# Optimization experiments

Measured on AMD Instinct MI355X. Metric: run time of the kernel, lower is better.

## Reference

```python
import jax, jax.numpy as jnp
import numpy as np
from jax import lax

B = 16384
BN_EPS = 1e-5


def setup_inputs() -> dict:
    key = jax.random.key(0)
    ks = jax.random.split(key, 6)
    x = jax.random.normal(ks[0], (B, 1, 28, 28), jnp.float32)
    conv_w = jax.random.normal(ks[1], (4, 1, 3, 3), jnp.float32) * 0.2
    bn_gamma = jnp.ones((4,), jnp.float32)
    bn_beta = jnp.zeros((4,), jnp.float32)
    bn_mean = jnp.zeros((4,), jnp.float32)
    bn_var = jnp.ones((4,), jnp.float32)
    var_params = jax.random.normal(ks[2], (4,), jnp.float32)
    lin_w = jax.random.normal(ks[3], (10, 784), jnp.float32) * 0.03
    lin_b = jnp.zeros((10,), jnp.float32)
    return {"x": x, "conv_w": conv_w, "bn_gamma": bn_gamma, "bn_beta": bn_beta,
            "bn_mean": bn_mean, "bn_var": bn_var, "var_params": var_params,
            "lin_w": lin_w, "lin_b": lin_b}


def _ry_w0(s, theta):
    # apply RY(theta) to wire 0 (axis -2) of real state s[..., 2, 2]
    c, si = jnp.cos(theta * 0.5), jnp.sin(theta * 0.5)
    R = jnp.stack([jnp.stack([c, -si]), jnp.stack([si, c])])
    return jnp.einsum('ij,...jk->...ik', R, s)


def _ry_w1(s, theta):
    # apply RY(theta) to wire 1 (axis -1)
    c, si = jnp.cos(theta * 0.5), jnp.sin(theta * 0.5)
    R = jnp.stack([jnp.stack([c, -si]), jnp.stack([si, c])])
    return jnp.einsum('ij,...kj->...ki', R, s)


def _quantum_features(img, v):
    # img: [B, 28, 28] -> features [B, 196*4] (patch-major, 4 expvals each)
    b = img.shape[0]
    p = img.reshape(b, 14, 2, 14, 2).transpose(0, 1, 3, 2, 4)  # [B,14,14,2,2]
    # encoding RYs on same wire compose: angles a = p0+p2 (wire0), b = p1+p3 (wire1)
    ha = (p[..., 0, 0] + p[..., 1, 0]) * 0.5
    hb = (p[..., 0, 1] + p[..., 1, 1]) * 0.5
    w0 = jnp.stack([jnp.cos(ha), jnp.sin(ha)], axis=-1)
    w1 = jnp.stack([jnp.cos(hb), jnp.sin(hb)], axis=-1)
    s = w0[..., :, None] * w1[..., None, :]  # real statevector [B,14,14,2,2]
    # CNOT(control=0, target=1): flip wire1 where wire0 == 1
    s = jnp.stack([s[..., 0, :], s[..., 1, ::-1]], axis=-2)
    s = _ry_w0(s, v[0])
    s = _ry_w1(s, v[1])
    # CNOT(control=1, target=0): flip wire0 where wire1 == 1
    s = jnp.stack([s[..., :, 0], s[..., ::-1, 1]], axis=-1)
    s = _ry_w0(s, v[2])
    s = _ry_w1(s, v[3])
    z0 = jnp.sum(s[..., 0, :] ** 2 - s[..., 1, :] ** 2, axis=-1)
    z1 = jnp.sum(s[..., :, 0] ** 2 - s[..., :, 1] ** 2, axis=-1)
    x0 = 2.0 * jnp.sum(s[..., 0, :] * s[..., 1, :], axis=-1)
    x1 = 2.0 * jnp.sum(s[..., :, 0] * s[..., :, 1], axis=-1)
    return jnp.stack([z0, z1, x0, x1], axis=-1).reshape(b, -1)  # [B,784]


def reference(x, conv_w, bn_gamma, bn_beta, bn_mean, bn_var, var_params, lin_w, lin_b):
    b = x.shape[0]
    # classical branch: conv(s=2,p=1) -> BN (eval) -> ReLU -> flatten
    h = lax.conv_general_dilated(x, conv_w, window_strides=(2, 2),
                                 padding=((1, 1), (1, 1)))  # [B,4,14,14]
    inv = bn_gamma / jnp.sqrt(bn_var + BN_EPS)
    h = h * inv[None, :, None, None] + (bn_beta - bn_mean * inv)[None, :, None, None]
    h = jnp.maximum(h, 0.0)
    cls_out = h.reshape(b, -1)  # [B,784]
    # quantum branch over 2x2 patches
    q_out = _quantum_features(x[:, 0], var_params)  # [B,784]
    fused = cls_out + q_out
    logits = fused @ lin_w.T + lin_b
    return jax.nn.log_softmax(logits, axis=-1)
```

## Files before the change

kernel.cpp:

```cpp
#include <hip/hip_runtime.h>
#include <math.h>


#define NW 4
#define SCLS_STRIDE 794

typedef __fp16 h2 __attribute__((ext_vector_type(2)));
typedef __fp16 h4 __attribute__((ext_vector_type(4)));

#if __has_builtin(__builtin_amdgcn_fdot2)
#define FDOT2(a, b, c) __builtin_amdgcn_fdot2((a), (b), (c), false)
#else
__device__ __forceinline__ float FDOT2(h2 a, h2 b, float c) {
    return (float)a.x * (float)b.x + (float)a.y * (float)b.y + c;
}
#endif

__device__ __forceinline__ float2 red32x2(float x) {
    int v;
    v = __builtin_amdgcn_update_dpp(0, __float_as_int(x), 0x111, 0xf, 0xf, true); x += __int_as_float(v);
    v = __builtin_amdgcn_update_dpp(0, __float_as_int(x), 0x112, 0xf, 0xf, true); x += __int_as_float(v);
    v = __builtin_amdgcn_update_dpp(0, __float_as_int(x), 0x114, 0xf, 0xf, true); x += __int_as_float(v);
    v = __builtin_amdgcn_update_dpp(0, __float_as_int(x), 0x118, 0xf, 0xf, true); x += __int_as_float(v);
    v = __builtin_amdgcn_update_dpp(0, __float_as_int(x), 0x142, 0xa, 0xf, true); x += __int_as_float(v);
    float2 r;
    r.x = __int_as_float(__builtin_amdgcn_readlane(__float_as_int(x), 31));
    r.y = __int_as_float(__builtin_amdgcn_readlane(__float_as_int(x), 63));
    return r;
}

__global__ __launch_bounds__(256, 4)
void quanv_fused(const float* __restrict__ x,
                 const float* __restrict__ conv_w,
                 const float* __restrict__ bn_gamma,
                 const float* __restrict__ bn_beta,
                 const float* __restrict__ bn_mean,
                 const float* __restrict__ bn_var,
                 const float* __restrict__ var_params,
                 const float* __restrict__ lin_w,
                 const float* __restrict__ lin_b,
                 float* __restrict__ out, int B)
{
    __shared__ __align__(16) __fp16 lwh[7840];
    __shared__ __align__(16) __fp16 sclsAll[NW * 2 * SCLS_STRIDE];

    const int tid  = threadIdx.x;
    const int wave = tid >> 6;
    const int lane = tid & 63;
    const int half = lane >> 5;
    const int l32  = lane & 31;

    const int s  = blockIdx.x * (NW * 2) + wave * 2 + half;
    const int sc = (s < B) ? s : (B - 1);
    const float* xs = x + (size_t)sc * 784;
    __fp16* myscls = &sclsAll[(wave * 2 + half) * SCLS_STRIDE];

    {
        const float4* src = (const float4*)lin_w;
        #pragma unroll
        for (int t = 0; t < 8; ++t) {
            int i = tid + t * 256;
            if (i < 1960) {
                float4 v = src[i];
                h2 a = __builtin_amdgcn_cvt_pkrtz(v.x, v.y);
                h2 b = __builtin_amdgcn_cvt_pkrtz(v.z, v.w);
                h4 w4 = { a.x, a.y, b.x, b.y };
                *(h4*)&lwh[4 * i] = w4;
            }
        }
    }

    float w[36];
    #pragma unroll
    for (int k = 0; k < 36; ++k) w[k] = conv_w[k];
    float inv[4], addc[4];
    #pragma unroll
    for (int c = 0; c < 4; ++c) {
        float iv = bn_gamma[c] * rsqrtf(bn_var[c] + 1e-5f);
        inv[c]  = iv;
        addc[c] = bn_beta[c] - bn_mean[c] * iv;
    }
    float cv[4], sv[4];
    #pragma unroll
    for (int k = 0; k < 4; ++k) __sincosf(var_params[k] * 0.5f, &sv[k], &cv[k]);

    h2 qh[7][2];
    #pragma unroll
    for (int t = 0; t < 7; ++t) {
        int p = l32 + 32 * t;
        bool act = (p < 196);
        int pc = act ? p : 195;
        unsigned i = (unsigned)pc / 14u;
        int j = pc - (int)i * 14;
        int omid = (int)(2 * i) * 28 + 2 * j;

        float2 Rm = *(const float2*)(xs + omid);
        float2 Rb = *(const float2*)(xs + omid + 28);
        int ot = omid - 28; ot = (ot > 0) ? ot : 0;
        float2 Rt = *(const float2*)(xs + ot);
        int olt = omid - 30; olt = (olt > 0) ? olt : 0;
        float2 Lt = *(const float2*)(xs + olt);
        int olm = omid - 2; olm = (olm > 0) ? olm : 0;
        float2 Lm = *(const float2*)(xs + olm);
        float2 Lb = *(const float2*)(xs + olm + 28);

        float mt = (i > 0) ? 1.f : 0.f;
        float ml = (j > 0) ? 1.f : 0.f;
        float a00 = Lt.y * (mt * ml), a01 = Rt.x * mt, a02 = Rt.y * mt;
        float a10 = Lm.y * ml,        a11 = Rm.x,      a12 = Rm.y;
        float a20 = Lb.y * ml,        a21 = Rb.x,      a22 = Rb.y;

        if (act) {
            #pragma unroll
            for (int c = 0; c < 4; ++c) {
                float h = w[c*9+0]*a00 + w[c*9+1]*a01 + w[c*9+2]*a02
                        + w[c*9+3]*a10 + w[c*9+4]*a11 + w[c*9+5]*a12
                        + w[c*9+6]*a20 + w[c*9+7]*a21 + w[c*9+8]*a22;
                h = h * inv[c] + addc[c];
                myscls[c * 196 + pc] = (__fp16)fmaxf(h, 0.f);
            }
        }

        float ha = 0.5f * (a11 + a21);
        float hb = 0.5f * (a12 + a22);
        float c0, s0, c1, s1;
        __sincosf(ha, &s0, &c0);
        __sincosf(hb, &s1, &c1);
        float m00 = c0*c1, m01 = c0*s1;
        float m10 = s0*s1, m11 = s0*c1;
        float t00 = cv[0]*m00 - sv[0]*m10, t01 = cv[0]*m01 - sv[0]*m11;
        float t10 = sv[0]*m00 + cv[0]*m10, t11 = sv[0]*m01 + cv[0]*m11;
        float u00 = cv[1]*t00 - sv[1]*t01, u01 = sv[1]*t00 + cv[1]*t01;
        float u10 = cv[1]*t10 - sv[1]*t11, u11 = sv[1]*t10 + cv[1]*t11;
        float tmp = u01; u01 = u11; u11 = tmp;
        float p00 = cv[2]*u00 - sv[2]*u10, p01 = cv[2]*u01 - sv[2]*u11;
        float p10 = sv[2]*u00 + cv[2]*u10, p11 = sv[2]*u01 + cv[2]*u11;
        float q00 = cv[3]*p00 - sv[3]*p01, q01 = sv[3]*p00 + cv[3]*p01;
        float q10 = cv[3]*p10 - sv[3]*p11, q11 = sv[3]*p10 + cv[3]*p11;

        float z0 = q00*q00 + q01*q01 - q10*q10 - q11*q11;
        float z1 = q00*q00 + q10*q10 - q01*q01 - q11*q11;
        float x0 = 2.f * (q00*q10 + q01*q11);
        float x1 = 2.f * (q00*q01 + q10*q11);
        qh[t][0] = __builtin_amdgcn_cvt_pkrtz(z0, z1);
        qh[t][1] = __builtin_amdgcn_cvt_pkrtz(x0, x1);
    }

    __syncthreads();

    float ps[10];
    #pragma unroll
    for (int o = 0; o < 10; ++o) ps[o] = 0.f;

    const h2 hz = { (__fp16)0.f, (__fp16)0.f };
    #pragma unroll
    for (int t = 0; t < 7; ++t) {
        int p = l32 + 32 * t;
        bool act = (p < 196);
        int pc = act ? p : 195;
        h2 c0 = *(const h2*)&myscls[4 * pc];
        h2 c1 = *(const h2*)&myscls[4 * pc + 2];
        h2 f0 = c0 + qh[t][0];
        h2 f1 = c1 + qh[t][1];
        f0 = act ? f0 : hz;
        f1 = act ? f1 : hz;
        const __fp16* wbase = &lwh[4 * pc];
        #pragma unroll
        for (int o = 0; o < 10; ++o) {
            h4 wv = *(const h4*)&wbase[o * 784];
            h2 wlo = __builtin_shufflevector(wv, wv, 0, 1);
            h2 whi = __builtin_shufflevector(wv, wv, 2, 3);
            ps[o] = FDOT2(f0, wlo, ps[o]);
            ps[o] = FDOT2(f1, whi, ps[o]);
        }
    }

    float lg[10];
    #pragma unroll
    for (int o = 0; o < 10; ++o) {
        float2 r = red32x2(ps[o]);
        lg[o] = (half ? r.y : r.x) + lin_b[o];
    }

    float mx = lg[0];
    #pragma unroll
    for (int o = 1; o < 10; ++o) mx = fmaxf(mx, lg[o]);
    float se = 0.f;
    #pragma unroll
    for (int o = 0; o < 10; ++o) se += __expf(lg[o] - mx);
    float ls = __logf(se);

    int o32 = l32;
    if (o32 < 10 && s < B) {
        float v = lg[0];
        #pragma unroll
        for (int o = 1; o < 10; ++o) v = (o32 == o) ? lg[o] : v;
        out[(size_t)s * 10 + o32] = v - mx - ls;
    }
}

extern "C" void kernel_launch(void* const* d_in, const int* in_sizes, int n_in,
                              void* d_out, int out_size, void* d_ws, size_t ws_size,
                              hipStream_t stream) {
    const float* x          = (const float*)d_in[0];
    const float* conv_w     = (const float*)d_in[1];
    const float* bn_gamma   = (const float*)d_in[2];
    const float* bn_beta    = (const float*)d_in[3];
    const float* bn_mean    = (const float*)d_in[4];
    const float* bn_var     = (const float*)d_in[5];
    const float* var_params = (const float*)d_in[6];
    const float* lin_w      = (const float*)d_in[7];
    const float* lin_b      = (const float*)d_in[8];
    float* out = (float*)d_out;

    const int B = in_sizes[0] / 784;
    const int blocks = (B + NW * 2 - 1) / (NW * 2);
    quanv_fused<<<blocks, 256, 0, stream>>>(x, conv_w, bn_gamma, bn_beta, bn_mean,
                                            bn_var, var_params, lin_w, lin_b, out, B);
}
```

Measured before the change: 111.1 us.

## Use MFMA for the linear layer and precompute folded quantum coefficients

```diff
diff --git a/kernel.cpp b/kernel.cpp
--- a/kernel.cpp
+++ b/kernel.cpp
@@ -2,200 +2,233 @@
 #include <math.h>
 
 
-#define NW 4
-#define SCLS_STRIDE 794
-
 typedef __fp16 h2 __attribute__((ext_vector_type(2)));
 typedef __fp16 h4 __attribute__((ext_vector_type(4)));
-
-#if __has_builtin(__builtin_amdgcn_fdot2)
-#define FDOT2(a, b, c) __builtin_amdgcn_fdot2((a), (b), (c), false)
-#else
-__device__ __forceinline__ float FDOT2(h2 a, h2 b, float c) {
-    return (float)a.x * (float)b.x + (float)a.y * (float)b.y + c;
-}
-#endif
-
-__device__ __forceinline__ float2 red32x2(float x) {
-    int v;
-    v = __builtin_amdgcn_update_dpp(0, __float_as_int(x), 0x111, 0xf, 0xf, true); x += __int_as_float(v);
-    v = __builtin_amdgcn_update_dpp(0, __float_as_int(x), 0x112, 0xf, 0xf, true); x += __int_as_float(v);
-    v = __builtin_amdgcn_update_dpp(0, __float_as_int(x), 0x114, 0xf, 0xf, true); x += __int_as_float(v);
-    v = __builtin_amdgcn_update_dpp(0, __float_as_int(x), 0x118, 0xf, 0xf, true); x += __int_as_float(v);
-    v = __builtin_amdgcn_update_dpp(0, __float_as_int(x), 0x142, 0xa, 0xf, true); x += __int_as_float(v);
-    float2 r;
-    r.x = __int_as_float(__builtin_amdgcn_readlane(__float_as_int(x), 31));
-    r.y = __int_as_float(__builtin_amdgcn_readlane(__float_as_int(x), 63));
-    return r;
-}
-
-__global__ __launch_bounds__(256, 4)
-void quanv_fused(const float* __restrict__ x,
-                 const float* __restrict__ conv_w,
-                 const float* __restrict__ bn_gamma,
-                 const float* __restrict__ bn_beta,
-                 const float* __restrict__ bn_mean,
-                 const float* __restrict__ bn_var,
-                 const float* __restrict__ var_params,
-                 const float* __restrict__ lin_w,
-                 const float* __restrict__ lin_b,
-                 float* __restrict__ out, int B)
+typedef __fp16 h8 __attribute__((ext_vector_type(8)));
+typedef float f32x4 __attribute__((ext_vector_type(4)));
+
+#define NSAMP 16
+#define FSTRIDE 808
+
+__global__ void quanv_precomp(const float* __restrict__ conv_w,
+                              const float* __restrict__ bn_gamma,
+                              const float* __restrict__ bn_beta,
+                              const float* __restrict__ bn_mean,
+                              const float* __restrict__ bn_var,
+                              const float* __restrict__ var_params,
+                              float* __restrict__ ws)
 {
-    __shared__ __align__(16) __fp16 lwh[7840];
-    __shared__ __align__(16) __fp16 sclsAll[NW * 2 * SCLS_STRIDE];
-
-    const int tid  = threadIdx.x;
-    const int wave = tid >> 6;
-    const int lane = tid & 63;
-    const int half = lane >> 5;
-    const int l32  = lane & 31;
-
-    const int s  = blockIdx.x * (NW * 2) + wave * 2 + half;
-    const int sc = (s < B) ? s : (B - 1);
-    const float* xs = x + (size_t)sc * 784;
-    __fp16* myscls = &sclsAll[(wave * 2 + half) * SCLS_STRIDE];
-
-    {
-        const float4* src = (const float4*)lin_w;
-        #pragma unroll
-        for (int t = 0; t < 8; ++t) {
-            int i = tid + t * 256;
-            if (i < 1960) {
-                float4 v = src[i];
-                h2 a = __builtin_amdgcn_cvt_pkrtz(v.x, v.y);
-                h2 b = __builtin_amdgcn_cvt_pkrtz(v.z, v.w);
-                h4 w4 = { a.x, a.y, b.x, b.y };
-                *(h4*)&lwh[4 * i] = w4;
-            }
-        }
-    }
-
-    float w[36];
-    #pragma unroll
-    for (int k = 0; k < 36; ++k) w[k] = conv_w[k];
-    float inv[4], addc[4];
+    if (threadIdx.x != 0 || blockIdx.x != 0) return;
+
     #pragma unroll
     for (int c = 0; c < 4; ++c) {
         float iv = bn_gamma[c] * rsqrtf(bn_var[c] + 1e-5f);
-        inv[c]  = iv;
-        addc[c] = bn_beta[c] - bn_mean[c] * iv;
-    }
+        #pragma unroll
+        for (int k = 0; k < 9; ++k) ws[c * 9 + k] = conv_w[c * 9 + k] * iv;
+        ws[36 + c] = bn_beta[c] - bn_mean[c] * iv;
+    }
+
     float cv[4], sv[4];
     #pragma unroll
     for (int k = 0; k < 4; ++k) __sincosf(var_params[k] * 0.5f, &sv[k], &cv[k]);
 
-    h2 qh[7][2];
+    float U[4][4];
+    #pragma unroll
+    for (int col = 0; col < 4; ++col) {
+        float v0 = (col == 0), v1 = (col == 1), v2 = (col == 2), v3 = (col == 3);
+        float t;
+        t = v2; v2 = v3; v3 = t;
+        t = cv[0]*v0 - sv[0]*v2; v2 = sv[0]*v0 + cv[0]*v2; v0 = t;
+        t = cv[0]*v1 - sv[0]*v3; v3 = sv[0]*v1 + cv[0]*v3; v1 = t;
+        t = cv[1]*v0 - sv[1]*v1; v1 = sv[1]*v0 + cv[1]*v1; v0 = t;
+        t = cv[1]*v2 - sv[1]*v3; v3 = sv[1]*v2 + cv[1]*v3; v2 = t;
+        t = v1; v1 = v3; v3 = t;
+        t = cv[2]*v0 - sv[2]*v2; v2 = sv[2]*v0 + cv[2]*v2; v0 = t;
+        t = cv[2]*v1 - sv[2]*v3; v3 = sv[2]*v1 + cv[2]*v3; v1 = t;
+        t = cv[3]*v0 - sv[3]*v1; v1 = sv[3]*v0 + cv[3]*v1; v0 = t;
+        t = cv[3]*v2 - sv[3]*v3; v3 = sv[3]*v2 + cv[3]*v3; v2 = t;
+        U[0][col] = v0; U[1][col] = v1; U[2][col] = v2; U[3][col] = v3;
+    }
+
+    #pragma unroll
+    for (int f = 0; f < 4; ++f) {
+        float M[4][4];
+        #pragma unroll
+        for (int r = 0; r < 4; ++r) {
+            int src = r; float sgn = 1.f;
+            if      (f == 0) { sgn = (r < 2) ? 1.f : -1.f; }
+            else if (f == 1) { sgn = ((r & 1) == 0) ? 1.f : -1.f; }
+            else if (f == 2) { src = r ^ 2; }
+            else             { src = r ^ 1; }
+            #pragma unroll
+            for (int j = 0; j < 4; ++j) M[r][j] = sgn * U[src][j];
+        }
+        float A[4][4];
+        #pragma unroll
+        for (int i = 0; i < 4; ++i)
+            #pragma unroll
+            for (int j = 0; j < 4; ++j)
+                A[i][j] = U[0][i]*M[0][j] + U[1][i]*M[1][j]
+                        + U[2][i]*M[2][j] + U[3][i]*M[3][j];
+
+        float a1 = 0.5f*(A[0][0]+A[1][1]), b1 = 0.5f*(A[0][0]-A[1][1]), g1 = 0.5f*(A[0][1]+A[1][0]);
+        float a2 = 0.5f*(A[2][2]+A[3][3]), b2 = 0.5f*(A[2][2]-A[3][3]), g2 = 0.5f*(A[2][3]+A[3][2]);
+        float u00 = A[0][2]+A[2][0], u01 = A[0][3]+A[2][1];
+        float u10 = A[1][2]+A[3][0], u11 = A[1][3]+A[3][1];
+        float a3 = 0.5f*(u00+u11), b3 = 0.5f*(u00-u11), g3 = 0.5f*(u01+u10);
+
+        float* K = ws + 40 + 9 * f;
+        K[0] = 0.5f*(a1+a2); K[1] = 0.5f*(a1-a2); K[2] = 0.5f*a3;
+        K[3] = 0.5f*(b1+b2); K[4] = 0.5f*(b1-b2); K[5] = 0.5f*b3;
+        K[6] = 0.5f*(g1+g2); K[7] = 0.5f*(g1-g2); K[8] = 0.5f*g3;
+    }
+}
+
+__global__ __launch_bounds__(256, 3)
+void quanv_main(const float* __restrict__ x,
+                const float* __restrict__ ws,
+                const float* __restrict__ lin_w,
+                const float* __restrict__ lin_b,
+                float* __restrict__ out, int B)
+{
+    __shared__ __align__(16) __fp16 clsB[NSAMP * FSTRIDE];
+    __shared__ __align__(16) __fp16 qB[NSAMP * FSTRIDE];
+
+    const int tid  = threadIdx.x;
+    const int lane = tid & 63;
+    const int wave = tid >> 6;
+
+    {
+        int r = tid >> 4, buf = (tid >> 3) & 1, w = tid & 7;
+        int* wp = (int*)((buf ? qB : clsB) + r * FSTRIDE + 784);
+        wp[w] = 0;
+    }
+
+    const int bcol = lane & 15, bkg = lane >> 4;
+    const __fp16 hz = (__fp16)0.f;
+    h8 bfrag[7];
     #pragma unroll
     for (int t = 0; t < 7; ++t) {
-        int p = l32 + 32 * t;
-        bool act = (p < 196);
-        int pc = act ? p : 195;
-        unsigned i = (unsigned)pc / 14u;
-        int j = pc - (int)i * 14;
-        int omid = (int)(2 * i) * 28 + 2 * j;
-
-        float2 Rm = *(const float2*)(xs + omid);
-        float2 Rb = *(const float2*)(xs + omid + 28);
-        int ot = omid - 28; ot = (ot > 0) ? ot : 0;
+        int st = wave * 7 + t;
+        int kb = st * 32 + bkg * 8;
+        h8 bf = {hz, hz, hz, hz, hz, hz, hz, hz};
+        if (bcol < 10 && kb < 784) {
+            const float4* lw4 = (const float4*)(lin_w + bcol * 784 + kb);
+            float4 v0 = lw4[0], v1 = lw4[1];
+            h2 p0 = __builtin_amdgcn_cvt_pkrtz(v0.x, v0.y);
+            h2 p1 = __builtin_amdgcn_cvt_pkrtz(v0.z, v0.w);
+            h2 p2 = __builtin_amdgcn_cvt_pkrtz(v1.x, v1.y);
+            h2 p3 = __builtin_amdgcn_cvt_pkrtz(v1.z, v1.w);
+            h8 tv = {p0.x, p0.y, p1.x, p1.y, p2.x, p2.y, p3.x, p3.y};
+            bf = tv;
+        }
+        bfrag[t] = bf;
+    }
+
+    const int s_loc = tid >> 4;
+    const int pcol  = tid & 15;
+    const int sg    = blockIdx.x * NSAMP + s_loc;
+    const int sgc   = (sg < B) ? sg : (B - 1);
+    const float* xs = x + (size_t)sgc * 784;
+    __fp16* clsRow  = clsB + s_loc * FSTRIDE;
+    __fp16* qRow    = qB   + s_loc * FSTRIDE;
+
+    #pragma unroll
+    for (int it = 0; it < 13; ++it) {
+        int p = pcol + 16 * it;
+        p = (p < 196) ? p : 195;
+        unsigned ii = (unsigned)p / 14u;
+        int j  = p - (int)ii * 14;
+        int om = (int)ii * 56 + 2 * j;
+
+        float2 Rm = *(const float2*)(xs + om);
+        float2 Rb = *(const float2*)(xs + om + 28);
+        int ot = om - 28;  ot  = (ot  > 0) ? ot  : 0;
         float2 Rt = *(const float2*)(xs + ot);
-        int olt = omid - 30; olt = (olt > 0) ? olt : 0;
+        int olt = om - 30; olt = (olt > 0) ? olt : 0;
         float2 Lt = *(const float2*)(xs + olt);
-        int olm = omid - 2; olm = (olm > 0) ? olm : 0;
+        int olm = om - 2;  olm = (olm > 0) ? olm : 0;
         float2 Lm = *(const float2*)(xs + olm);
         float2 Lb = *(const float2*)(xs + olm + 28);
 
-        float mt = (i > 0) ? 1.f : 0.f;
-        float ml = (j > 0) ? 1.f : 0.f;
+        float mt = (ii > 0u) ? 1.f : 0.f;
+        float ml = (j  > 0 ) ? 1.f : 0.f;
         float a00 = Lt.y * (mt * ml), a01 = Rt.x * mt, a02 = Rt.y * mt;
         float a10 = Lm.y * ml,        a11 = Rm.x,      a12 = Rm.y;
         float a20 = Lb.y * ml,        a21 = Rb.x,      a22 = Rb.y;
 
-        if (act) {
-            #pragma unroll
-            for (int c = 0; c < 4; ++c) {
-                float h = w[c*9+0]*a00 + w[c*9+1]*a01 + w[c*9+2]*a02
-                        + w[c*9+3]*a10 + w[c*9+4]*a11 + w[c*9+5]*a12
-                        + w[c*9+6]*a20 + w[c*9+7]*a21 + w[c*9+8]*a22;
-                h = h * inv[c] + addc[c];
-                myscls[c * 196 + pc] = (__fp16)fmaxf(h, 0.f);
+        #pragma unroll
+        for (int c = 0; c < 4; ++c) {
+            float h = ws[36 + c];
+            h = fmaf(ws[c*9+0], a00, h); h = fmaf(ws[c*9+1], a01, h);
+            h = fmaf(ws[c*9+2], a02, h); h = fmaf(ws[c*9+3], a10, h);
+            h = fmaf(ws[c*9+4], a11, h); h = fmaf(ws[c*9+5], a12, h);
+            h = fmaf(ws[c*9+6], a20, h); h = fmaf(ws[c*9+7], a21, h);
+            h = fmaf(ws[c*9+8], a22, h);
+            clsRow[c * 196 + p] = (__fp16)fmaxf(h, 0.f);
+        }
+
+        float cA, sA, cB, sB;
+        __sincosf(a11 + a21, &sA, &cA);
+        __sincosf(a12 + a22, &sB, &cB);
+        float o[4];
+        #pragma unroll
+        for (int f = 0; f < 4; ++f) {
+            const float* k = ws + 40 + 9 * f;
+            float t1 = fmaf(k[2], sA, fmaf(k[1], cA, k[0]));
+            float t2 = fmaf(k[5], sA, fmaf(k[4], cA, k[3]));
+            float t3 = fmaf(k[8], sA, fmaf(k[7], cA, k[6]));
+            o[f] = fmaf(t3, sB, fmaf(t2, cB, t1));
+        }
+        h2 zz = __builtin_amdgcn_cvt_pkrtz(o[0], o[1]);
+        h2 xx = __builtin_amdgcn_cvt_pkrtz(o[2], o[3]);
+        h4 qv = {zz.x, zz.y, xx.x, xx.y};
+        *(h4*)(qRow + 4 * p) = qv;
+    }
+
+    __syncthreads();
+
+    f32x4 acc = {0.f, 0.f, 0.f, 0.f};
+    {
+        const int arow = lane & 15, akg = lane >> 4;
+        #pragma unroll
+        for (int t = 0; t < 7; ++t) {
+            int st = wave * 7 + t;
+            if (st < 25) {
+                int off = arow * FSTRIDE + st * 32 + akg * 8;
+                h8 a = *(const h8*)(clsB + off) + *(const h8*)(qB + off);
+                acc = __builtin_amdgcn_mfma_f32_16x16x32_f16(a, bfrag[t], acc, 0, 0, 0);
             }
         }
-
-        float ha = 0.5f * (a11 + a21);
-        float hb = 0.5f * (a12 + a22);
-        float c0, s0, c1, s1;
-        __sincosf(ha, &s0, &c0);
-        __sincosf(hb, &s1, &c1);
-        float m00 = c0*c1, m01 = c0*s1;
-        float m10 = s0*s1, m11 = s0*c1;
-        float t00 = cv[0]*m00 - sv[0]*m10, t01 = cv[0]*m01 - sv[0]*m11;
-        float t10 = sv[0]*m00 + cv[0]*m10, t11 = sv[0]*m01 + cv[0]*m11;
-        float u00 = cv[1]*t00 - sv[1]*t01, u01 = sv[1]*t00 + cv[1]*t01;
-        float u10 = cv[1]*t10 - sv[1]*t11, u11 = sv[1]*t10 + cv[1]*t11;
-        float tmp = u01; u01 = u11; u11 = tmp;
-        float p00 = cv[2]*u00 - sv[2]*u10, p01 = cv[2]*u01 - sv[2]*u11;
-        float p10 = sv[2]*u00 + cv[2]*u10, p11 = sv[2]*u01 + cv[2]*u11;
-        float q00 = cv[3]*p00 - sv[3]*p01, q01 = sv[3]*p00 + cv[3]*p01;
-        float q10 = cv[3]*p10 - sv[3]*p11, q11 = sv[3]*p10 + cv[3]*p11;
-
-        float z0 = q00*q00 + q01*q01 - q10*q10 - q11*q11;
-        float z1 = q00*q00 + q10*q10 - q01*q01 - q11*q11;
-        float x0 = 2.f * (q00*q10 + q01*q11);
-        float x1 = 2.f * (q00*q01 + q10*q11);
-        qh[t][0] = __builtin_amdgcn_cvt_pkrtz(z0, z1);
-        qh[t][1] = __builtin_amdgcn_cvt_pkrtz(x0, x1);
     }
 
     __syncthreads();
-
-    float ps[10];
-    #pragma unroll
-    for (int o = 0; o < 10; ++o) ps[o] = 0.f;
-
-    const h2 hz = { (__fp16)0.f, (__fp16)0.f };
-    #pragma unroll
-    for (int t = 0; t < 7; ++t) {
-        int p = l32 + 32 * t;
-        bool act = (p < 196);
-        int pc = act ? p : 195;
-        h2 c0 = *(const h2*)&myscls[4 * pc];
-        h2 c1 = *(const h2*)&myscls[4 * pc + 2];
-        h2 f0 = c0 + qh[t][0];
-        h2 f1 = c1 + qh[t][1];
-        f0 = act ? f0 : hz;
-        f1 = act ? f1 : hz;
-        const __fp16* wbase = &lwh[4 * pc];
-        #pragma unroll
-        for (int o = 0; o < 10; ++o) {
-            h4 wv = *(const h4*)&wbase[o * 784];
-            h2 wlo = __builtin_shufflevector(wv, wv, 0, 1);
-            h2 whi = __builtin_shufflevector(wv, wv, 2, 3);
-            ps[o] = FDOT2(f0, wlo, ps[o]);
-            ps[o] = FDOT2(f1, whi, ps[o]);
-        }
-    }
-
-    float lg[10];
-    #pragma unroll
-    for (int o = 0; o < 10; ++o) {
-        float2 r = red32x2(ps[o]);
-        lg[o] = (half ? r.y : r.x) + lin_b[o];
-    }
-
-    float mx = lg[0];
-    #pragma unroll
-    for (int o = 1; o < 10; ++o) mx = fmaxf(mx, lg[o]);
-    float se = 0.f;
-    #pragma unroll
-    for (int o = 0; o < 10; ++o) se += __expf(lg[o] - mx);
-    float ls = __logf(se);
-
-    int o32 = l32;
-    if (o32 < 10 && s < B) {
-        float v = lg[0];
-        #pragma unroll
-        for (int o = 1; o < 10; ++o) v = (o32 == o) ? lg[o] : v;
-        out[(size_t)s * 10 + o32] = v - mx - ls;
+    float* pw = (float*)clsB;
+    {
+        const int col = lane & 15, rb = (lane >> 4) * 4;
+        #pragma unroll
+        for (int r = 0; r < 4; ++r)
+            pw[(wave * 16 + rb + r) * 16 + col] = acc[r];
+    }
+    __syncthreads();
+
+    {
+        const int c = tid & 15;
+        float L = pw[s_loc * 16 + c] + pw[(16 + s_loc) * 16 + c]
+                + pw[(32 + s_loc) * 16 + c] + pw[(48 + s_loc) * 16 + c];
+        L = (c < 10) ? (L + lin_b[c]) : -1e30f;
+        float mx = L;
+        mx = fmaxf(mx, __shfl_xor(mx, 1, 16));
+        mx = fmaxf(mx, __shfl_xor(mx, 2, 16));
+        mx = fmaxf(mx, __shfl_xor(mx, 4, 16));
+        mx = fmaxf(mx, __shfl_xor(mx, 8, 16));
+        float se = (c < 10) ? __expf(L - mx) : 0.f;
+        se += __shfl_xor(se, 1, 16);
+        se += __shfl_xor(se, 2, 16);
+        se += __shfl_xor(se, 4, 16);
+        se += __shfl_xor(se, 8, 16);
+        if (c < 10 && sg < B)
+            out[(size_t)sg * 10 + c] = L - mx - __logf(se);
     }
 }
 
@@ -212,9 +245,11 @@
     const float* lin_w      = (const float*)d_in[7];
     const float* lin_b      = (const float*)d_in[8];
     float* out = (float*)d_out;
+    float* ws  = (float*)d_ws;
 
     const int B = in_sizes[0] / 784;
-    const int blocks = (B + NW * 2 - 1) / (NW * 2);
-    quanv_fused<<<blocks, 256, 0, stream>>>(x, conv_w, bn_gamma, bn_beta, bn_mean,
-                                            bn_var, var_params, lin_w, lin_b, out, B);
+    quanv_precomp<<<1, 64, 0, stream>>>(conv_w, bn_gamma, bn_beta, bn_mean,
+                                        bn_var, var_params, ws);
+    const int blocks = (B + NSAMP - 1) / NSAMP;
+    quanv_main<<<blocks, 256, 0, stream>>>(x, ws, lin_w, lin_b, out, B);
 }
```

Result: slower. 124.2 us (+11.7%).
